# Optimization experiments

Measured on AMD Instinct MI355X. Metric: run time of the kernel, lower is better.

Reference implementation:

```python
import jax, jax.numpy as jnp
import numpy as np

EPS = 1e-8  # torch CosineSimilarity default eps


def setup_inputs() -> dict:
    key = jax.random.key(0)
    k_emb, k_idx, k_w1, k_w2 = jax.random.split(key, 4)
    N, H, E = 50000, 128, 800000
    emb = jax.random.normal(k_emb, (N, H), dtype=jnp.float32)
    edge_index = jax.random.randint(k_idx, (2, E), 0, N, dtype=jnp.int64)
    # xavier_uniform for square H x H: limit = sqrt(6 / (H + H))
    lim = float(np.sqrt(6.0 / (H + H)))
    W1 = jax.random.uniform(k_w1, (H, H), dtype=jnp.float32, minval=-lim, maxval=lim)
    W2 = jax.random.uniform(k_w2, (H, H), dtype=jnp.float32, minval=-lim, maxval=lim)
    b1 = jnp.zeros((H,), dtype=jnp.float32)
    b2 = jnp.zeros((H,), dtype=jnp.float32)
    return {"emb": emb, "edge_index": edge_index, "W1": W1, "b1": b1, "W2": W2, "b2": b2}


def reference(emb, edge_index, W1, b1, W2, b2):
    col, row = edge_index[0], edge_index[1]

    def mlp(x):  # Linear -> (Dropout: identity at eval) -> ELU -> Linear
        h = jax.nn.elu(x @ W1.T + b1)
        return h @ W2.T + b2

    f1 = mlp(emb[col])  # [E, H]
    f2 = mlp(emb[row])  # [E, H]
    n1 = jnp.maximum(jnp.sqrt(jnp.sum(f1 * f1, axis=1)), EPS)
    n2 = jnp.maximum(jnp.sqrt(jnp.sum(f2 * f2, axis=1)), EPS)
    return jnp.sum(f1 * f2, axis=1) / (n1 * n2)  # [E]
```

## Files before the change

kernel.cpp:

```cpp
#include <hip/hip_runtime.h>
#include <math.h>

#define H 128
#define MROWS 64
#define XS 136

#if defined(__has_builtin)
# if __has_builtin(__builtin_amdgcn_sdot4)
#  define HAVE_SDOT4 1
# endif
#endif

typedef __attribute__((ext_vector_type(8))) short short8;
typedef __attribute__((ext_vector_type(4))) float floatx4;

__device__ __forceinline__ unsigned short f2bf(float f) {
    unsigned u = __float_as_uint(f);
    return (unsigned short)((u + 0x7FFFu + ((u >> 16) & 1u)) >> 16);
}

__global__ void prep_weights(const float* __restrict__ W1,
                             const float* __restrict__ W2,
                             unsigned short* __restrict__ Wbf) {
    int i = blockIdx.x * 256 + threadIdx.x;
    if (i < 16384)       Wbf[i] = f2bf(W1[i]);
    else if (i < 32768)  Wbf[i] = f2bf(W2[i - 16384]);
}

__global__ __launch_bounds__(256, 2) void mlp_mfma(
    const float* __restrict__ emb, const unsigned short* __restrict__ Wbf,
    const float* __restrict__ b1, const float* __restrict__ b2,
    signed char* __restrict__ qtab, float* __restrict__ scl, int N)
{
    __shared__ unsigned short Wl[H * XS];
    __shared__ unsigned short xs[MROWS * XS];
    __shared__ unsigned short hs[MROWS * XS];

    const int tid   = threadIdx.x;
    const int wave  = tid >> 6, lane = tid & 63;
    const int quad  = lane >> 4, l15 = lane & 15;
    const int node0 = blockIdx.x * MROWS;

    {
        const float4* src = (const float4*)Wbf;
        #pragma unroll
        for (int i = 0; i < 8; ++i) {
            int cc = i * 256 + tid;
            int row = cc >> 4, c = cc & 15;
            *(float4*)(Wl + row * XS + c * 8) = src[cc];
        }
    }
    #pragma unroll
    for (int i = 0; i < 8; ++i) {
        int flat = i * 1024 + tid * 4;
        int rowl = flat >> 7, col = flat & 127;
        float4 v = make_float4(0.f, 0.f, 0.f, 0.f);
        if (node0 + rowl < N)
            v = *(const float4*)(emb + (size_t)(node0 + rowl) * H + col);
        ushort4 b;
        b.x = f2bf(v.x); b.y = f2bf(v.y); b.z = f2bf(v.z); b.w = f2bf(v.w);
        *(ushort4*)(xs + rowl * XS + col) = b;
    }
    __syncthreads();

    const int mrow = wave * 16 + l15;
    short8 afr[4];

    #pragma unroll
    for (int ks = 0; ks < 4; ++ks)
        afr[ks] = *(const short8*)(xs + mrow * XS + ks * 32 + quad * 8);
    #pragma unroll
    for (int nt = 0; nt < 8; ++nt) {
        floatx4 acc = {0.f, 0.f, 0.f, 0.f};
        #pragma unroll
        for (int ks = 0; ks < 4; ++ks) {
            short8 bfr = *(const short8*)(Wl + (nt * 16 + l15) * XS + ks * 32 + quad * 8);
            acc = __builtin_amdgcn_mfma_f32_16x16x32_bf16(afr[ks], bfr, acc, 0, 0, 0);
        }
        const int col = nt * 16 + l15;
        const float bb1 = b1[col];
        #pragma unroll
        for (int r = 0; r < 4; ++r) {
            float v = acc[r] + bb1;
            v = v > 0.f ? v : (__expf(v) - 1.f);
            hs[(wave * 16 + quad * 4 + r) * XS + col] = f2bf(v);
        }
    }
    __syncthreads();

    #pragma unroll
    for (int ks = 0; ks < 4; ++ks)
        afr[ks] = *(const short8*)(hs + mrow * XS + ks * 32 + quad * 8);
    {
        const float4* src = (const float4*)(Wbf + 16384);
        #pragma unroll
        for (int i = 0; i < 8; ++i) {
            int cc = i * 256 + tid;
            int row = cc >> 4, c = cc & 15;
            *(float4*)(Wl + row * XS + c * 8) = src[cc];
        }
    }
    __syncthreads();

    floatx4 av[8];
    float sq[4] = {0.f, 0.f, 0.f, 0.f};
    float am[4] = {0.f, 0.f, 0.f, 0.f};
    #pragma unroll
    for (int nt = 0; nt < 8; ++nt) {
        floatx4 acc = {0.f, 0.f, 0.f, 0.f};
        #pragma unroll
        for (int ks = 0; ks < 4; ++ks) {
            short8 bfr = *(const short8*)(Wl + (nt * 16 + l15) * XS + ks * 32 + quad * 8);
            acc = __builtin_amdgcn_mfma_f32_16x16x32_bf16(afr[ks], bfr, acc, 0, 0, 0);
        }
        const float bb2 = b2[nt * 16 + l15];
        #pragma unroll
        for (int r = 0; r < 4; ++r) {
            float v = acc[r] + bb2;
            av[nt][r] = v;
            sq[r] += v * v;
            am[r] = fmaxf(am[r], fabsf(v));
        }
    }
    #pragma unroll
    for (int r = 0; r < 4; ++r) {
        float s = sq[r], a = am[r];
        #pragma unroll
        for (int m = 8; m; m >>= 1) {
            s += __shfl_xor(s, m);
            a = fmaxf(a, __shfl_xor(a, m));
        }
        sq[r] = s; am[r] = a;
    }
    #pragma unroll
    for (int r = 0; r < 4; ++r) {
        const int row = wave * 16 + quad * 4 + r;
        const int G = node0 + row;
        if (G < N) {
            const float a = fmaxf(am[r], 1e-20f);
            if (l15 == 0) {
                float nn = sqrtf(sq[r]);
                if (nn < 1e-8f) nn = 1e-8f;
                scl[G] = a / (nn * 127.f);
            }
            const float qs = 127.f / a;
            unsigned pk0 = 0, pk1 = 0;
            #pragma unroll
            for (int nt = 0; nt < 4; ++nt) {
                int q = (int)rintf(av[nt][r] * qs);
                q = q > 127 ? 127 : (q < -127 ? -127 : q);
                pk0 |= ((unsigned)(q & 255)) << (8 * nt);
            }
            #pragma unroll
            for (int nt = 4; nt < 8; ++nt) {
                int q = (int)rintf(av[nt][r] * qs);
                q = q > 127 ? 127 : (q < -127 ? -127 : q);
                pk1 |= ((unsigned)(q & 255)) << (8 * (nt - 4));
            }
            *(uint2*)(qtab + (size_t)G * H + l15 * 8) = make_uint2(pk0, pk1);
        }
    }
}

__device__ __forceinline__ int dot4s(unsigned a, unsigned b) {
    int s = 0;
    #pragma unroll
    for (int j = 0; j < 4; ++j)
        s += (int)((signed char)(a >> (8 * j))) * (int)((signed char)(b >> (8 * j)));
    return s;
}

__device__ __forceinline__ int dot16(uint4 a, uint4 b) {
#if defined(HAVE_SDOT4)
    int s = __builtin_amdgcn_sdot4((int)a.x, (int)b.x, 0, false);
    s = __builtin_amdgcn_sdot4((int)a.y, (int)b.y, s, false);
    s = __builtin_amdgcn_sdot4((int)a.z, (int)b.z, s, false);
    s = __builtin_amdgcn_sdot4((int)a.w, (int)b.w, s, false);
    return s;
#else
    return dot4s(a.x, b.x) + dot4s(a.y, b.y) + dot4s(a.z, b.z) + dot4s(a.w, b.w);
#endif
}

__global__ __launch_bounds__(256) void edge_cos(
    const int* __restrict__ ei, const signed char* __restrict__ qtab,
    const float* __restrict__ scl, float* __restrict__ out, int E)
{
    const int tid = threadIdx.x;
    const int sub = tid & 7;
    const int g   = (blockIdx.x * 256 + tid) >> 3;
    const int e0  = g * 4;
    if (e0 >= E) return;

    int cc[4], rr[4];
    #pragma unroll
    for (int k = 0; k < 4; ++k) {
        int e = e0 + k;
        if (e >= E) e = E - 1;
        cc[k] = __builtin_nontemporal_load(ei + e);
        rr[k] = __builtin_nontemporal_load(ei + e + E);
    }
    uint4 ua[4], ub[4];
    #pragma unroll
    for (int k = 0; k < 4; ++k) {
        ua[k] = *(const uint4*)(qtab + (size_t)cc[k] * H + sub * 16);
        ub[k] = *(const uint4*)(qtab + (size_t)rr[k] * H + sub * 16);
    }
    float sc[4];
    #pragma unroll
    for (int k = 0; k < 4; ++k) sc[k] = scl[cc[k]] * scl[rr[k]];

    #pragma unroll
    for (int k = 0; k < 4; ++k) {
        int s = dot16(ua[k], ub[k]);
        s += __shfl_xor(s, 4);
        s += __shfl_xor(s, 2);
        s += __shfl_xor(s, 1);
        if (sub == 0 && e0 + k < E)
            __builtin_nontemporal_store((float)s * sc[k], out + e0 + k);
    }
}

extern "C" void kernel_launch(void* const* d_in, const int* in_sizes, int n_in,
                              void* d_out, int out_size, void* d_ws, size_t ws_size,
                              hipStream_t stream) {
    const float* emb = (const float*)d_in[0];
    const int*   ei  = (const int*)d_in[1];
    const float* W1  = (const float*)d_in[2];
    const float* b1  = (const float*)d_in[3];
    const float* W2  = (const float*)d_in[4];
    const float* b2  = (const float*)d_in[5];
    float*       out = (float*)d_out;

    const int N = in_sizes[0] / H;
    const int E = in_sizes[1] / 2;

    unsigned short* Wbf  = (unsigned short*)d_ws;
    signed char*    qtab = (signed char*)(Wbf + 32768);
    float*          sclp = (float*)(qtab + (size_t)N * H);

    prep_weights<<<128, 256, 0, stream>>>(W1, W2, Wbf);
    mlp_mfma<<<(N + MROWS - 1) / MROWS, 256, 0, stream>>>(emb, Wbf, b1, b2, qtab, sclp, N);
    edge_cos<<<(E + 127) / 128, 256, 0, stream>>>(ei, qtab, sclp, out, E);
}
```

Baseline: 121.5 us.

## Fuse weight bf16 conversion into MLP kernel and load emb directly to registers

Removes the separate prep_weights launch: each MLP block now reads fp32 W1/W2 and converts them to bf16 while staging into LDS. Embedding rows are loaded straight from global memory into MFMA A-fragments, which removes the xs LDS buffer and one LDS round trip. The lower LDS footprint allows the launch bound to request 3 blocks per SM. In exchange, every block reads twice as many weight bytes (fp32 instead of bf16) and redoes the conversion, and the per-lane emb loads are less coalesced.

```diff
diff --git a/kernel.cpp b/kernel.cpp
--- a/kernel.cpp
+++ b/kernel.cpp
@@ -19,21 +19,13 @@
     return (unsigned short)((u + 0x7FFFu + ((u >> 16) & 1u)) >> 16);
 }
 
-__global__ void prep_weights(const float* __restrict__ W1,
-                             const float* __restrict__ W2,
-                             unsigned short* __restrict__ Wbf) {
-    int i = blockIdx.x * 256 + threadIdx.x;
-    if (i < 16384)       Wbf[i] = f2bf(W1[i]);
-    else if (i < 32768)  Wbf[i] = f2bf(W2[i - 16384]);
-}
-
-__global__ __launch_bounds__(256, 2) void mlp_mfma(
-    const float* __restrict__ emb, const unsigned short* __restrict__ Wbf,
-    const float* __restrict__ b1, const float* __restrict__ b2,
+__global__ __launch_bounds__(256, 3) void mlp_mfma(
+    const float* __restrict__ emb, const float* __restrict__ W1,
+    const float* __restrict__ W2, const float* __restrict__ b1,
+    const float* __restrict__ b2,
     signed char* __restrict__ qtab, float* __restrict__ scl, int N)
 {
     __shared__ unsigned short Wl[H * XS];
-    __shared__ unsigned short xs[MROWS * XS];
     __shared__ unsigned short hs[MROWS * XS];
 
     const int tid   = threadIdx.x;
@@ -41,34 +33,39 @@
     const int quad  = lane >> 4, l15 = lane & 15;
     const int node0 = blockIdx.x * MROWS;
 
-    {
-        const float4* src = (const float4*)Wbf;
-        #pragma unroll
-        for (int i = 0; i < 8; ++i) {
-            int cc = i * 256 + tid;
-            int row = cc >> 4, c = cc & 15;
-            *(float4*)(Wl + row * XS + c * 8) = src[cc];
-        }
-    }
-    #pragma unroll
-    for (int i = 0; i < 8; ++i) {
-        int flat = i * 1024 + tid * 4;
-        int rowl = flat >> 7, col = flat & 127;
-        float4 v = make_float4(0.f, 0.f, 0.f, 0.f);
-        if (node0 + rowl < N)
-            v = *(const float4*)(emb + (size_t)(node0 + rowl) * H + col);
+    const int  mrow = wave * 16 + l15;
+    const int  grow = node0 + mrow;
+    const bool rv   = grow < N;
+
+    #pragma unroll
+    for (int i = 0; i < 16; ++i) {
+        int f = i * 1024 + tid * 4;
+        int row = f >> 7, c = f & 127;
+        float4 v = *(const float4*)(W1 + f);
         ushort4 b;
         b.x = f2bf(v.x); b.y = f2bf(v.y); b.z = f2bf(v.z); b.w = f2bf(v.w);
-        *(ushort4*)(xs + rowl * XS + col) = b;
+        *(ushort4*)(Wl + row * XS + c) = b;
+    }
+
+    short8 afr[4];
+    #pragma unroll
+    for (int ks = 0; ks < 4; ++ks) {
+        float4 u0 = make_float4(0.f, 0.f, 0.f, 0.f);
+        float4 u1 = make_float4(0.f, 0.f, 0.f, 0.f);
+        if (rv) {
+            const float* p = emb + (size_t)grow * H + ks * 32 + quad * 8;
+            u0 = *(const float4*)p;
+            u1 = *(const float4*)(p + 4);
+        }
+        short8 a;
+        a[0] = (short)f2bf(u0.x); a[1] = (short)f2bf(u0.y);
+        a[2] = (short)f2bf(u0.z); a[3] = (short)f2bf(u0.w);
+        a[4] = (short)f2bf(u1.x); a[5] = (short)f2bf(u1.y);
+        a[6] = (short)f2bf(u1.z); a[7] = (short)f2bf(u1.w);
+        afr[ks] = a;
     }
     __syncthreads();
 
-    const int mrow = wave * 16 + l15;
-    short8 afr[4];
-
-    #pragma unroll
-    for (int ks = 0; ks < 4; ++ks)
-        afr[ks] = *(const short8*)(xs + mrow * XS + ks * 32 + quad * 8);
     #pragma unroll
     for (int nt = 0; nt < 8; ++nt) {
         floatx4 acc = {0.f, 0.f, 0.f, 0.f};
@@ -91,14 +88,14 @@
     #pragma unroll
     for (int ks = 0; ks < 4; ++ks)
         afr[ks] = *(const short8*)(hs + mrow * XS + ks * 32 + quad * 8);
-    {
-        const float4* src = (const float4*)(Wbf + 16384);
-        #pragma unroll
-        for (int i = 0; i < 8; ++i) {
-            int cc = i * 256 + tid;
-            int row = cc >> 4, c = cc & 15;
-            *(float4*)(Wl + row * XS + c * 8) = src[cc];
-        }
+    #pragma unroll
+    for (int i = 0; i < 16; ++i) {
+        int f = i * 1024 + tid * 4;
+        int row = f >> 7, c = f & 127;
+        float4 v = *(const float4*)(W2 + f);
+        ushort4 b;
+        b.x = f2bf(v.x); b.y = f2bf(v.y); b.z = f2bf(v.z); b.w = f2bf(v.w);
+        *(ushort4*)(Wl + row * XS + c) = b;
     }
     __syncthreads();
 
@@ -235,11 +232,10 @@
     const int N = in_sizes[0] / H;
     const int E = in_sizes[1] / 2;
 
-    unsigned short* Wbf  = (unsigned short*)d_ws;
-    signed char*    qtab = (signed char*)(Wbf + 32768);
-    float*          sclp = (float*)(qtab + (size_t)N * H);
-
-    prep_weights<<<128, 256, 0, stream>>>(W1, W2, Wbf);
-    mlp_mfma<<<(N + MROWS - 1) / MROWS, 256, 0, stream>>>(emb, Wbf, b1, b2, qtab, sclp, N);
+    signed char* qtab = (signed char*)d_ws;
+    float*       sclp = (float*)(qtab + (size_t)N * H);
+
+    mlp_mfma<<<(N + MROWS - 1) / MROWS, 256, 0, stream>>>(emb, W1, W2, b1, b2,
+                                                          qtab, sclp, N);
     edge_cos<<<(E + 127) / 128, 256, 0, stream>>>(ei, qtab, sclp, out, E);
 }
```

After: 119.8 us. Within noise of the previous version (-1.4%).
